# Performance work log

Hardware: AMD Instinct MI355X
Metric: run time of the kernel (lower is better)

The kernel has to match this reference:

```python
import jax, jax.numpy as jnp
import numpy as np

B, T, IN_CH, FIRST_CH, BLOCK_CH, SCALED_CH, K, ND = 8, 16384, 256, 256, 24, 128, 2, 10


def _conv1d(x, W, b, d=1):
    # x: (B, L, Cin), W: (K, Cin, Cout), keras Conv1D with padding='valid'
    y = jax.lax.conv_general_dilated(x, W, (1,), 'VALID', rhs_dilation=(d,),
                                     dimension_numbers=('NWC', 'WIO', 'NWC'))
    return y + b


def _gated(x, gW, gb, fW, fb, sW, sb, d):
    g = jax.nn.sigmoid(_conv1d(x, gW, gb, d))
    f = jnp.tanh(_conv1d(x, fW, fb, d))
    return _conv1d(f * g, sW, sb, 1)


def setup_inputs():
    key = jax.random.key(0)
    ks = jax.random.split(key, 11)
    s = 0.1
    n9 = ND - 1  # blocks 1..9 share channel count BLOCK_CH -> stacked weights
    return {
        'x': jax.random.normal(ks[0], (B, T, IN_CH), jnp.float32),
        'causal_W': jax.random.normal(ks[1], (K, IN_CH, FIRST_CH)) * s,
        'causal_b': jnp.zeros((FIRST_CH,)),
        'gW0': jax.random.normal(ks[2], (K, FIRST_CH, BLOCK_CH)) * s,
        'gb0': jnp.zeros((BLOCK_CH,)),
        'fW0': jax.random.normal(ks[3], (K, FIRST_CH, BLOCK_CH)) * s,
        'fb0': jnp.zeros((BLOCK_CH,)),
        'sW0': jax.random.normal(ks[4], (1, BLOCK_CH, BLOCK_CH)) * s,
        'sb0': jnp.zeros((BLOCK_CH,)),
        'gate_W': jax.random.normal(ks[5], (n9, K, BLOCK_CH, BLOCK_CH)) * s,
        'gate_b': jnp.zeros((n9, BLOCK_CH)),
        'filter_W': jax.random.normal(ks[6], (n9, K, BLOCK_CH, BLOCK_CH)) * s,
        'filter_b': jnp.zeros((n9, BLOCK_CH)),
        'scale_W': jax.random.normal(ks[7], (n9, 1, BLOCK_CH, BLOCK_CH)) * s,
        'scale_b': jnp.zeros((n9, BLOCK_CH)),
        'res_W': jax.random.normal(ks[8], (n9, 1, BLOCK_CH, SCALED_CH)) * s,
        'res_b': jnp.zeros((n9, SCALED_CH)),
        'f1_W': jax.random.normal(ks[9], (1, SCALED_CH, IN_CH)) * s,
        'f1_b': jnp.zeros((IN_CH,)),
        'f2_W': jax.random.normal(ks[10], (1, IN_CH, IN_CH)) * s,
        'f2_b': jnp.zeros((IN_CH,)),
    }


def reference(x, causal_W, causal_b, gW0, gb0, fW0, fb0, sW0, sb0,
              gate_W, gate_b, filter_W, filter_b, scale_W, scale_b,
              res_W, res_b, f1_W, f1_b, f2_W, f2_b):
    out = _conv1d(x, causal_W, causal_b)  # (B, T-1, 256)
    # block 0 (dilation 1): prev_in has 256 ch vs 24 ch out -> residual branch skipped
    out = _gated(out, gW0, gb0, fW0, fb0, sW0, sb0, 1)
    acc = None
    for i in range(ND - 1):
        d = 2 ** (i + 1)  # even -> trim d//2 on each side
        prev = out
        out = _gated(prev, gate_W[i], gate_b[i], filter_W[i], filter_b[i],
                     scale_W[i], scale_b[i], d)
        trimmed = prev[:, d // 2: prev.shape[1] - d // 2, :]
        # NOTE: original code OVERWRITES the accumulator each iteration
        acc = _conv1d(trimmed + out, res_W[i], res_b[i], 1)
    a = jax.nn.relu(acc)  # (B, 15360, 128)
    a = jax.nn.relu(_conv1d(a, f1_W, f1_b, 1))  # (B, 15360, 256)
    return jax.nn.softmax(_conv1d(a, f2_W, f2_b, 1), axis=-1)
```

## Files before the change

kernel.cpp:

```cpp
#include <hip/hip_runtime.h>
#include <math.h>

typedef unsigned short u16;
typedef __attribute__((ext_vector_type(8))) short short8;
typedef __attribute__((ext_vector_type(4))) float f32x4;

#define PBSTR ((long)16382 * 24)

__device__ __forceinline__ u16 f2bf(float f) {
    unsigned u = __float_as_uint(f);
    unsigned r = u + 0x7FFFu + ((u >> 16) & 1u);
    return (u16)(r >> 16);
}
__device__ __forceinline__ unsigned pk2(float a, float b) {
    return (unsigned)f2bf(a) | ((unsigned)f2bf(b) << 16);
}
__device__ __forceinline__ float sigf(float x) { return 1.f / (1.f + __expf(-x)); }
__device__ __forceinline__ float tanhfast(float x) { return 2.f / (1.f + __expf(-2.f * x)) - 1.f; }

__device__ __forceinline__ short8 ldfrag(const u16* p) { return *(const short8*)p; }
__device__ __forceinline__ short8 ldfrag(const float* p) {
    float4 v0 = *(const float4*)p;
    float4 v1 = *(const float4*)(p + 4);
    union { uint4 u; short8 s; } cv;
    cv.u.x = pk2(v0.x, v0.y); cv.u.y = pk2(v0.z, v0.w);
    cv.u.z = pk2(v1.x, v1.y); cv.u.w = pk2(v1.z, v1.w);
    return cv.s;
}

__global__ __launch_bounds__(256) void build_gf_w(
    const float* __restrict__ cW, const float* __restrict__ cb,
    const float* __restrict__ gW, const float* __restrict__ gb,
    const float* __restrict__ fW, const float* __restrict__ fb,
    u16* __restrict__ Wt, float* __restrict__ biasGF)
{
    int idx = blockIdx.x * 256 + threadIdx.x;
    if (idx < 49152) {
        int nr = idx / 768, k = idx % 768, tau = k / 256, ci = k % 256;
        float val = 0.f;
        if (nr < 48) {
            const float* G = (nr < 24) ? gW : fW;
            int n = (nr < 24) ? nr : nr - 24;
            auto dotf = [&](int i, int j) {
                const float* a = cW + i * 65536 + ci * 256;
                const float* g = G + j * 6144 + n;
                float s = 0.f;
                for (int o = 0; o < 256; ++o) s += a[o] * g[o * 24];
                return s;
            };
            if (tau == 0)      val = dotf(0, 0);
            else if (tau == 1) val = dotf(0, 1) + dotf(1, 0);
            else               val = dotf(1, 1);
        }
        Wt[idx] = f2bf(val);
    }
    if (blockIdx.x == 0 && threadIdx.x < 48) {
        int nr = threadIdx.x;
        const float* G = (nr < 24) ? gW : fW;
        const float* B = (nr < 24) ? gb : fb;
        int n = (nr < 24) ? nr : nr - 24;
        float s = B[n];
        for (int o = 0; o < 256; ++o) s += cb[o] * (G[o * 24 + n] + G[6144 + o * 24 + n]);
        biasGF[nr] = s;
    }
}

__global__ __launch_bounds__(256) void build_wt_misc(
    const float* __restrict__ f1W, const float* __restrict__ f2W,
    const float* __restrict__ resW8,
    const float* __restrict__ gateW, const float* __restrict__ filtW,
    const float* __restrict__ sclW,
    u16* __restrict__ Wt1, u16* __restrict__ Wt2, u16* __restrict__ Wtr,
    u16* __restrict__ Wgf, u16* __restrict__ Wsc)
{
    int idx = blockIdx.x * 256 + threadIdx.x;
    if (idx < 32768) {
        int n = idx / 128, k = idx % 128;
        Wt1[idx] = f2bf(f1W[k * 256 + n]);
    } else if (idx < 98304) {
        int j = idx - 32768; int n = j / 256, k = j % 256;
        Wt2[j] = f2bf(f2W[k * 256 + n]);
    } else if (idx < 102400) {
        int j = idx - 98304; int n = j / 32, k = j % 32;
        Wtr[j] = (k < 24) ? f2bf(resW8[k * 128 + n]) : (u16)0;
    } else if (idx < 130048) {
        int j = idx - 102400;
        int i = j / 3072, r = (j % 3072) / 64, k = j % 64;
        float v = 0.f;
        int tap = -1, ci = 0;
        if (k < 24) { tap = 0; ci = k; }
        else if (k >= 32 && k < 56) { tap = 1; ci = k - 32; }
        if (tap >= 0) {
            const float* W = (r < 24) ? gateW : filtW;
            int co = (r < 24) ? r : r - 24;
            v = W[((i * 2 + tap) * 24 + ci) * 24 + co];
        }
        Wgf[j] = f2bf(v);
    } else if (idx < 139264) {
        int j = idx - 130048;
        int i = j / 1024, r = (j % 1024) / 32, k = j % 32;
        float v = (r < 24 && k < 24) ? sclW[(i * 24 + k) * 24 + r] : 0.f;
        Wsc[j] = f2bf(v);
    }
}

template<typename AT, int KTOT, int NTILES, int ACT>
__global__ __launch_bounds__(256) void gemm_bstat(
    const AT* __restrict__ A, long A_bstride, int A_rs,
    const u16* __restrict__ Wt, int Wt_rs,
    const float* __restrict__ bias,
    u16* __restrict__ C, long C_bstride, int C_rs, int L_out)
{
    constexpr int BS = KTOT + 8;
    constexpr int NROWS = NTILES * 16;
    __shared__ __align__(16) u16 Bs[NROWS * BS];
    __shared__ float biasL[NROWS];
    const int tid = threadIdx.x;
    const int n0 = blockIdx.y * NROWS;

    for (int i = tid; i < NROWS * (KTOT / 8); i += 256) {
        int rn = i / (KTOT / 8), kk = i % (KTOT / 8);
        *(uint4*)&Bs[rn * BS + kk * 8] = *(const uint4*)(Wt + (long)(n0 + rn) * Wt_rs + kk * 8);
    }
    if (tid < NROWS) biasL[tid] = bias[n0 + tid];

    const int wv = tid >> 6, lane = tid & 63, col = lane & 15, quad = lane >> 4;
    const int b = blockIdx.z;
    const int m0 = blockIdx.x * 128 + wv * 32;
    const AT* Ab = A + (long)b * A_bstride;
    const int rmax = L_out - 1;

    f32x4 acc[2][NTILES];
#pragma unroll
    for (int i = 0; i < 2; ++i)
#pragma unroll
        for (int j = 0; j < NTILES; ++j) acc[i][j] = (f32x4){0.f, 0.f, 0.f, 0.f};

    __syncthreads();

#pragma unroll
    for (int k0 = 0; k0 < KTOT; k0 += 32) {
        short8 a[2];
#pragma unroll
        for (int mt = 0; mt < 2; ++mt) {
            int r = m0 + mt * 16 + col;
            if (r > rmax) r = rmax;
            a[mt] = ldfrag(Ab + (long)r * A_rs + k0 + quad * 8);
        }
#pragma unroll
        for (int nt = 0; nt < NTILES; ++nt) {
            short8 bb = *(const short8*)&Bs[(nt * 16 + col) * BS + k0 + quad * 8];
            acc[0][nt] = __builtin_amdgcn_mfma_f32_16x16x32_bf16(a[0], bb, acc[0][nt], 0, 0, 0);
            acc[1][nt] = __builtin_amdgcn_mfma_f32_16x16x32_bf16(a[1], bb, acc[1][nt], 0, 0, 0);
        }
    }

#pragma unroll
    for (int mt = 0; mt < 2; ++mt)
#pragma unroll
        for (int nt = 0; nt < NTILES; ++nt)
#pragma unroll
            for (int rr = 0; rr < 4; ++rr) {
                int t = m0 + mt * 16 + quad * 4 + rr;
                if (t < L_out) {
                    float v = acc[mt][nt][rr] + biasL[nt * 16 + col];
                    if (ACT == 1) v = fmaxf(v, 0.f);
                    C[(long)b * C_bstride + (long)t * C_rs + n0 + nt * 16 + col] = f2bf(v);
                }
            }
}

__global__ __launch_bounds__(256) void gf_fused_v3(
    const float* __restrict__ x, const u16* __restrict__ Wt,
    const float* __restrict__ biasGF,
    const float* __restrict__ sW, const float* __restrict__ sb,
    float* __restrict__ P)
{
    __shared__ __align__(16) union {
        u16 bs[48 * 392];
        struct { float pre[128 * 49]; float h[128 * 24]; } ep;
    } U;
    __shared__ float WsT[24 * 28];
    __shared__ float biasL[48];
    __shared__ float sbL[24];

    const int tid = threadIdx.x;
    const int m0 = blockIdx.x * 128;
    const int b = blockIdx.z;
    const float* xb = x + (long)b * (16384 * 256);
    const int L = 16382;

    for (int i = tid; i < 576; i += 256) { int c = i / 24, n = i % 24; WsT[n * 28 + c] = sW[i]; }
    if (tid < 48) biasL[tid] = biasGF[tid];
    if (tid < 24) sbL[tid] = sb[tid];

    const int wv = tid >> 6, lane = tid & 63, col = lane & 15, quad = lane >> 4;

    f32x4 acc[2][3];
#pragma unroll
    for (int i = 0; i < 2; ++i)
#pragma unroll
        for (int j = 0; j < 3; ++j) acc[i][j] = (f32x4){0.f, 0.f, 0.f, 0.f};

    for (int half = 0; half < 2; ++half) {
        if (half) __syncthreads();
        for (int i = tid; i < 2304; i += 256) {
            int rn = i / 48, kk = i % 48;
            *(uint4*)&U.bs[rn * 392 + kk * 8] =
                *(const uint4*)(Wt + (long)rn * 768 + half * 384 + kk * 8);
        }
        __syncthreads();

        for (int k0 = 0; k0 < 384; k0 += 32) {
            short8 a[2];
#pragma unroll
            for (int mt = 0; mt < 2; ++mt) {
                int g = m0 + wv * 32 + mt * 16 + col;
                if (g > 16381) g = 16381;
                a[mt] = ldfrag(xb + (long)g * 256 + half * 384 + k0 + quad * 8);
            }
#pragma unroll
            for (int nt = 0; nt < 3; ++nt) {
                short8 bb = *(const short8*)&U.bs[(nt * 16 + col) * 392 + k0 + quad * 8];
                acc[0][nt] = __builtin_amdgcn_mfma_f32_16x16x32_bf16(a[0], bb, acc[0][nt], 0, 0, 0);
                acc[1][nt] = __builtin_amdgcn_mfma_f32_16x16x32_bf16(a[1], bb, acc[1][nt], 0, 0, 0);
            }
        }
    }

    __syncthreads();
#pragma unroll
    for (int mt = 0; mt < 2; ++mt)
#pragma unroll
        for (int nt = 0; nt < 3; ++nt)
#pragma unroll
            for (int rr = 0; rr < 4; ++rr) {
                int lrow = wv * 32 + mt * 16 + quad * 4 + rr;
                int c = nt * 16 + col;
                U.ep.pre[lrow * 49 + c] = acc[mt][nt][rr] + biasL[c];
            }
    __syncthreads();
    for (int i = tid; i < 3072; i += 256) {
        int t = i / 24, c = i - t * 24;
        U.ep.h[t * 24 + c] = sigf(U.ep.pre[t * 49 + c]) * tanhfast(U.ep.pre[t * 49 + 24 + c]);
    }
    __syncthreads();
    {
        int t = tid >> 1, half = tid & 1;
        float hv[24];
#pragma unroll
        for (int q = 0; q < 6; ++q) {
            float4 v = *(const float4*)&U.ep.h[t * 24 + q * 4];
            hv[q * 4] = v.x; hv[q * 4 + 1] = v.y; hv[q * 4 + 2] = v.z; hv[q * 4 + 3] = v.w;
        }
        if (m0 + t < L) {
#pragma unroll
            for (int j = 0; j < 12; ++j) {
                int n = half * 12 + j;
                float o = sbL[n];
#pragma unroll
                for (int q = 0; q < 6; ++q) {
                    float4 w = *(const float4*)&WsT[n * 28 + q * 4];
                    o += hv[q*4] * w.x + hv[q*4+1] * w.y + hv[q*4+2] * w.z + hv[q*4+3] * w.w;
                }
                P[(long)b * PBSTR + (long)(m0 + t) * 24 + n] = o;
            }
        }
    }
}

__global__ __launch_bounds__(256) void gated_mfma(
    const float* __restrict__ Pin,
    const u16* __restrict__ WgfG, const float* __restrict__ gb,
    const float* __restrict__ fb,
    const u16* __restrict__ WsG, const float* __restrict__ sb,
    float* __restrict__ Q, int Lin, int Lout, int d, int trimOff)
{
    __shared__ __align__(16) union {
        u16 T[64 * 72];
        float pre[64 * 49];
    } U;
    __shared__ __align__(16) u16 Wgf[48 * 72];
    __shared__ __align__(16) u16 Ws[32 * 40];
    __shared__ __align__(16) u16 H[64 * 40];

    const int tid = threadIdx.x;
    const int m0 = blockIdx.x * 64;
    const int b = blockIdx.z;
    const float* Pb = Pin + (long)b * PBSTR;

    if (tid < 128) {
        int r = tid & 63, tap = tid >> 6;
        int t = m0 + r; if (t > Lout - 1) t = Lout - 1;
        const float* src = Pb + (long)(t + tap * d) * 24;
        u16* dst = &U.T[r * 72 + tap * 32];
#pragma unroll
        for (int q = 0; q < 3; ++q) {
            float4 va = *(const float4*)(src + q * 8);
            float4 vb = *(const float4*)(src + q * 8 + 4);
            uint4 u;
            u.x = pk2(va.x, va.y); u.y = pk2(va.z, va.w);
            u.z = pk2(vb.x, vb.y); u.w = pk2(vb.z, vb.w);
            *(uint4*)(dst + q * 8) = u;
        }
        *(uint4*)(dst + 24) = (uint4){0, 0, 0, 0};
    } else {
        for (int j = tid - 128; j < 384; j += 128) {
            int rn = j >> 3, kk = j & 7;
            *(uint4*)&Wgf[rn * 72 + kk * 8] = *(const uint4*)(WgfG + rn * 64 + kk * 8);
        }
        {
            int j = tid - 128;
            int rn = j >> 2, kk = j & 3;
            *(uint4*)&Ws[rn * 40 + kk * 8] = *(const uint4*)(WsG + rn * 32 + kk * 8);
        }
    }

    const int wv = tid >> 6, lane = tid & 63, col = lane & 15, quad = lane >> 4;

    __syncthreads();

    short8 bgf[2][3];
#pragma unroll
    for (int ks = 0; ks < 2; ++ks)
#pragma unroll
        for (int nt = 0; nt < 3; ++nt)
            bgf[ks][nt] = *(const short8*)&Wgf[(nt * 16 + col) * 72 + ks * 32 + quad * 8];

    short8 a0 = *(const short8*)&U.T[(wv * 16 + col) * 72 + quad * 8];
    short8 a1 = *(const short8*)&U.T[(wv * 16 + col) * 72 + 32 + quad * 8];

    f32x4 acc[3];
#pragma unroll
    for (int nt = 0; nt < 3; ++nt) acc[nt] = (f32x4){0.f, 0.f, 0.f, 0.f};
#pragma unroll
    for (int nt = 0; nt < 3; ++nt) {
        acc[nt] = __builtin_amdgcn_mfma_f32_16x16x32_bf16(a0, bgf[0][nt], acc[nt], 0, 0, 0);
        acc[nt] = __builtin_amdgcn_mfma_f32_16x16x32_bf16(a1, bgf[1][nt], acc[nt], 0, 0, 0);
    }

    __syncthreads();

    float bnt[3];
#pragma unroll
    for (int nt = 0; nt < 3; ++nt) {
        int n = nt * 16 + col;
        bnt[nt] = (n < 24) ? gb[n] : fb[n - 24];
    }
#pragma unroll
    for (int nt = 0; nt < 3; ++nt)
#pragma unroll
        for (int rr = 0; rr < 4; ++rr)
            U.pre[(wv * 16 + quad * 4 + rr) * 49 + nt * 16 + col] = acc[nt][rr] + bnt[nt];
    __syncthreads();

    for (int i2 = tid; i2 < 1536; i2 += 256) {
        int t = i2 / 24, c = i2 - t * 24;
        float g = U.pre[t * 49 + c], f = U.pre[t * 49 + 24 + c];
        H[t * 40 + c] = f2bf(sigf(g) * tanhfast(f));
    }
    for (int i2 = tid; i2 < 512; i2 += 256) {
        int t = i2 >> 3, c = i2 & 7;
        H[t * 40 + 24 + c] = 0;
    }
    __syncthreads();

    short8 aH = *(const short8*)&H[(wv * 16 + col) * 40 + quad * 8];
    f32x4 acc2[2];
#pragma unroll
    for (int nt = 0; nt < 2; ++nt) acc2[nt] = (f32x4){0.f, 0.f, 0.f, 0.f};
#pragma unroll
    for (int nt = 0; nt < 2; ++nt) {
        short8 bs2 = *(const short8*)&Ws[(nt * 16 + col) * 40 + quad * 8];
        acc2[nt] = __builtin_amdgcn_mfma_f32_16x16x32_bf16(aH, bs2, acc2[nt], 0, 0, 0);
    }

#pragma unroll
    for (int nt = 0; nt < 2; ++nt) {
        int n = nt * 16 + col;
        if (n < 24) {
            float sbn = sb[n];
#pragma unroll
            for (int rr = 0; rr < 4; ++rr) {
                int t = m0 + wv * 16 + quad * 4 + rr;
                if (t < Lout) {
                    float v = acc2[nt][rr] + sbn;
                    if (trimOff >= 0) v += Pb[(long)(t + trimOff) * 24 + n];
                    Q[(long)b * PBSTR + (long)t * 24 + n] = v;
                }
            }
        }
    }
}

__global__ __launch_bounds__(256) void f2_softmax_v2(
    const u16* __restrict__ A, const u16* __restrict__ Wt2,
    const float* __restrict__ bias, float* __restrict__ out)
{
    __shared__ __align__(16) u16 Bs[2][256 * 40];
    __shared__ float biasL[256];
    const int tid = threadIdx.x;
    const int b = blockIdx.y;
    const int t0 = blockIdx.x * 64;
    biasL[tid] = bias[tid];

    const int wv = tid >> 6, lane = tid & 63, col = lane & 15, quad = lane >> 4;
    const u16* Ab = A + (long)b * (15360L * 256);
    const int row = t0 + wv * 16 + col;

    auto stage = [&](int kc, int buf) {
#pragma unroll
        for (int j = 0; j < 4; ++j) {
            int idx = tid * 4 + j;
            int rn = idx >> 2, kk = idx & 3;
            *(uint4*)&Bs[buf][rn * 40 + kk * 8] =
                *(const uint4*)(Wt2 + (long)rn * 256 + kc * 32 + kk * 8);
        }
    };

    short8 afr[8];
#pragma unroll
    for (int kc = 0; kc < 8; ++kc)
        afr[kc] = *(const short8*)(Ab + (long)row * 256 + kc * 32 + quad * 8);

    f32x4 acc[16];
#pragma unroll
    for (int i = 0; i < 16; ++i) acc[i] = (f32x4){0.f, 0.f, 0.f, 0.f};

    stage(0, 0);
    __syncthreads();
    for (int kc = 0; kc < 8; ++kc) {
        int buf = kc & 1;
        if (kc < 7) stage(kc + 1, buf ^ 1);
#pragma unroll
        for (int nt = 0; nt < 16; ++nt) {
            short8 bb = *(const short8*)&Bs[buf][(nt * 16 + col) * 40 + quad * 8];
            acc[nt] = __builtin_amdgcn_mfma_f32_16x16x32_bf16(afr[kc], bb, acc[nt], 0, 0, 0);
        }
        __syncthreads();
    }

#pragma unroll
    for (int r = 0; r < 4; ++r) {
        int tl = wv * 16 + quad * 4 + r;
        float v[16];
        float m = -1e30f;
#pragma unroll
        for (int nt = 0; nt < 16; ++nt) {
            v[nt] = acc[nt][r] + biasL[nt * 16 + col];
            m = fmaxf(m, v[nt]);
        }
        m = fmaxf(m, __shfl_xor(m, 1));
        m = fmaxf(m, __shfl_xor(m, 2));
        m = fmaxf(m, __shfl_xor(m, 4));
        m = fmaxf(m, __shfl_xor(m, 8));
        float s = 0.f;
#pragma unroll
        for (int nt = 0; nt < 16; ++nt) { v[nt] = __expf(v[nt] - m); s += v[nt]; }
        s += __shfl_xor(s, 1);
        s += __shfl_xor(s, 2);
        s += __shfl_xor(s, 4);
        s += __shfl_xor(s, 8);
        float inv = 1.f / s;
        float* op = out + ((long)b * 15360 + t0 + tl) * 256;
#pragma unroll
        for (int nt = 0; nt < 16; ++nt) op[nt * 16 + col] = v[nt] * inv;
    }
}

extern "C" void kernel_launch(void* const* d_in, const int* in_sizes, int n_in,
                              void* d_out, int out_size, void* d_ws, size_t ws_size,
                              hipStream_t stream)
{
    const float* x        = (const float*)d_in[0];
    const float* causal_W = (const float*)d_in[1];
    const float* causal_b = (const float*)d_in[2];
    const float* gW0      = (const float*)d_in[3];
    const float* gb0      = (const float*)d_in[4];
    const float* fW0      = (const float*)d_in[5];
    const float* fb0      = (const float*)d_in[6];
    const float* sW0      = (const float*)d_in[7];
    const float* sb0      = (const float*)d_in[8];
    const float* gate_W   = (const float*)d_in[9];
    const float* gate_b   = (const float*)d_in[10];
    const float* filter_W = (const float*)d_in[11];
    const float* filter_b = (const float*)d_in[12];
    const float* scale_W  = (const float*)d_in[13];
    const float* scale_b  = (const float*)d_in[14];
    const float* res_W    = (const float*)d_in[15];
    const float* res_b    = (const float*)d_in[16];
    const float* f1_W     = (const float*)d_in[17];
    const float* f1_b     = (const float*)d_in[18];
    const float* f2_W     = (const float*)d_in[19];
    const float* f2_b     = (const float*)d_in[20];

    char* w = (char*)d_ws;
    u16* ACC  = (u16*)w;   w += (size_t)8 * 15360 * 128 * 2;
    u16* A1   = (u16*)w;   w += (size_t)8 * 15360 * 256 * 2;
    float* P0 = (float*)w; w += (size_t)8 * 16382 * 24 * 4;
    float* P1 = (float*)w; w += (size_t)8 * 16382 * 24 * 4;
    u16* WtGF = (u16*)w;   w += (size_t)64 * 768 * 2;
    u16* Wt1  = (u16*)w;   w += (size_t)256 * 128 * 2;
    u16* Wt2  = (u16*)w;   w += (size_t)256 * 256 * 2;
    u16* Wtr  = (u16*)w;   w += (size_t)128 * 32 * 2;
    float* biasGF = (float*)w; w += 256;
    u16* WgfG = (u16*)w;   w += (size_t)9 * 48 * 64 * 2;
    u16* WsG  = (u16*)w;   w += (size_t)9 * 32 * 32 * 2;

    dim3 blk(256);

    build_gf_w<<<dim3(192), blk, 0, stream>>>(causal_W, causal_b, gW0, gb0, fW0, fb0,
                                              WtGF, biasGF);
    build_wt_misc<<<dim3(544), blk, 0, stream>>>(f1_W, f2_W, res_W + (size_t)8 * 24 * 128,
                                                 gate_W, filter_W, scale_W,
                                                 Wt1, Wt2, Wtr, WgfG, WsG);

    gf_fused_v3<<<dim3(128, 1, 8), blk, 0, stream>>>(x, WtGF, biasGF, sW0, sb0, P0);

    float* Pprev = P0;
    float* Pnext = P1;
    int Lprev = 16382;
    for (int i = 0; i < 9; ++i) {
        int d = 2 << i;
        int L = Lprev - d;
        int trim = (i == 8) ? d / 2 : -1;
        gated_mfma<<<dim3((L + 63) / 64, 1, 8), blk, 0, stream>>>(
            Pprev, WgfG + (size_t)i * 3072, gate_b + i * 24, filter_b + i * 24,
            WsG + (size_t)i * 1024, scale_b + i * 24,
            Pnext, Lprev, L, d, trim);
        float* tmp = Pprev; Pprev = Pnext; Pnext = tmp;
        Lprev = L;
    }

    gemm_bstat<float, 32, 8, 1><<<dim3(120, 1, 8), blk, 0, stream>>>(
        Pprev, PBSTR, 24, Wtr, 32, res_b + 8 * 128,
        ACC, (long)15360 * 128, 128, 15360);

    gemm_bstat<u16, 128, 8, 1><<<dim3(120, 2, 8), blk, 0, stream>>>(
        ACC, (long)15360 * 128, 128, Wt1, 128, f1_b,
        A1, (long)15360 * 256, 256, 15360);

    f2_softmax_v2<<<dim3(240, 8), blk, 0, stream>>>(A1, Wt2, f2_b, (float*)d_out);
}
```

Measured before the change: 577.5 us.

## Store gated-block intermediates as bf16 and prefetch A fragments in GEMMs

The 24-channel intermediate buffers P0/P1 passed between the gated blocks now hold bf16 instead of fp32. Every gated block reads them with plain vector copies into shared memory instead of converting from fp32, which halves intermediate traffic. The first fused kernel double-buffers its fp32 x loads in registers ahead of the MFMA loop, and gemm_bstat loads all A fragments up front before the MFMA loop. The cost is an extra bf16 rounding on each residual path across ten chained layers, plus higher register pressure from the prefetch buffers.

```diff
diff --git a/kernel.cpp b/kernel.cpp
--- a/kernel.cpp
+++ b/kernel.cpp
@@ -12,6 +12,7 @@
     unsigned r = u + 0x7FFFu + ((u >> 16) & 1u);
     return (u16)(r >> 16);
 }
+__device__ __forceinline__ float bf2f(u16 v) { return __uint_as_float((unsigned)v << 16); }
 __device__ __forceinline__ unsigned pk2(float a, float b) {
     return (unsigned)f2bf(a) | ((unsigned)f2bf(b) << 16);
 }
@@ -25,6 +26,12 @@
     union { uint4 u; short8 s; } cv;
     cv.u.x = pk2(v0.x, v0.y); cv.u.y = pk2(v0.z, v0.w);
     cv.u.z = pk2(v1.x, v1.y); cv.u.w = pk2(v1.z, v1.w);
+    return cv.s;
+}
+__device__ __forceinline__ short8 cvt8(float4 lo, float4 hi) {
+    union { uint4 u; short8 s; } cv;
+    cv.u.x = pk2(lo.x, lo.y); cv.u.y = pk2(lo.z, lo.w);
+    cv.u.z = pk2(hi.x, hi.y); cv.u.w = pk2(hi.z, hi.w);
     return cv.s;
 }
 
@@ -113,6 +120,7 @@
 {
     constexpr int BS = KTOT + 8;
     constexpr int NROWS = NTILES * 16;
+    constexpr int KS = KTOT / 32;
     __shared__ __align__(16) u16 Bs[NROWS * BS];
     __shared__ float biasL[NROWS];
     const int tid = threadIdx.x;
@@ -130,28 +138,31 @@
     const AT* Ab = A + (long)b * A_bstride;
     const int rmax = L_out - 1;
 
-    f32x4 acc[2][NTILES];
-#pragma unroll
-    for (int i = 0; i < 2; ++i)
-#pragma unroll
-        for (int j = 0; j < NTILES; ++j) acc[i][j] = (f32x4){0.f, 0.f, 0.f, 0.f};
-
-    __syncthreads();
-
-#pragma unroll
-    for (int k0 = 0; k0 < KTOT; k0 += 32) {
-        short8 a[2];
+    short8 afr[KS][2];
+#pragma unroll
+    for (int ks = 0; ks < KS; ++ks)
 #pragma unroll
         for (int mt = 0; mt < 2; ++mt) {
             int r = m0 + mt * 16 + col;
             if (r > rmax) r = rmax;
-            a[mt] = ldfrag(Ab + (long)r * A_rs + k0 + quad * 8);
-        }
+            afr[ks][mt] = ldfrag(Ab + (long)r * A_rs + ks * 32 + quad * 8);
+        }
+
+    f32x4 acc[2][NTILES];
+#pragma unroll
+    for (int i = 0; i < 2; ++i)
+#pragma unroll
+        for (int j = 0; j < NTILES; ++j) acc[i][j] = (f32x4){0.f, 0.f, 0.f, 0.f};
+
+    __syncthreads();
+
+#pragma unroll
+    for (int ks = 0; ks < KS; ++ks) {
 #pragma unroll
         for (int nt = 0; nt < NTILES; ++nt) {
-            short8 bb = *(const short8*)&Bs[(nt * 16 + col) * BS + k0 + quad * 8];
-            acc[0][nt] = __builtin_amdgcn_mfma_f32_16x16x32_bf16(a[0], bb, acc[0][nt], 0, 0, 0);
-            acc[1][nt] = __builtin_amdgcn_mfma_f32_16x16x32_bf16(a[1], bb, acc[1][nt], 0, 0, 0);
+            short8 bb = *(const short8*)&Bs[(nt * 16 + col) * BS + ks * 32 + quad * 8];
+            acc[0][nt] = __builtin_amdgcn_mfma_f32_16x16x32_bf16(afr[ks][0], bb, acc[0][nt], 0, 0, 0);
+            acc[1][nt] = __builtin_amdgcn_mfma_f32_16x16x32_bf16(afr[ks][1], bb, acc[1][nt], 0, 0, 0);
         }
     }
 
@@ -170,11 +181,11 @@
             }
 }
 
-__global__ __launch_bounds__(256) void gf_fused_v3(
+__global__ __launch_bounds__(256) void gf_fused_v4(
     const float* __restrict__ x, const u16* __restrict__ Wt,
     const float* __restrict__ biasGF,
     const float* __restrict__ sW, const float* __restrict__ sb,
-    float* __restrict__ P)
+    u16* __restrict__ P)
 {
     __shared__ __align__(16) union {
         u16 bs[48 * 392];
@@ -196,12 +207,34 @@
 
     const int wv = tid >> 6, lane = tid & 63, col = lane & 15, quad = lane >> 4;
 
+    long rowoff[2];
+#pragma unroll
+    for (int mt = 0; mt < 2; ++mt) {
+        int g = m0 + wv * 32 + mt * 16 + col;
+        if (g > 16381) g = 16381;
+        rowoff[mt] = (long)g * 256 + quad * 8;
+    }
+
+    float4 pf[2][2][2];
+    auto loadA = [&](int kk, int slot) {
+#pragma unroll
+        for (int mt = 0; mt < 2; ++mt) {
+            const float* p = xb + rowoff[mt] + kk * 32;
+            pf[slot][mt][0] = *(const float4*)p;
+            pf[slot][mt][1] = *(const float4*)(p + 4);
+        }
+    };
+
     f32x4 acc[2][3];
 #pragma unroll
     for (int i = 0; i < 2; ++i)
 #pragma unroll
         for (int j = 0; j < 3; ++j) acc[i][j] = (f32x4){0.f, 0.f, 0.f, 0.f};
 
+    loadA(0, 0);
+    loadA(1, 1);
+
+#pragma unroll
     for (int half = 0; half < 2; ++half) {
         if (half) __syncthreads();
         for (int i = tid; i < 2304; i += 256) {
@@ -211,19 +244,18 @@
         }
         __syncthreads();
 
-        for (int k0 = 0; k0 < 384; k0 += 32) {
-            short8 a[2];
-#pragma unroll
-            for (int mt = 0; mt < 2; ++mt) {
-                int g = m0 + wv * 32 + mt * 16 + col;
-                if (g > 16381) g = 16381;
-                a[mt] = ldfrag(xb + (long)g * 256 + half * 384 + k0 + quad * 8);
-            }
+#pragma unroll
+        for (int s = 0; s < 12; ++s) {
+            const int kk = half * 12 + s;
+            const int slot = s & 1;
+            short8 a0 = cvt8(pf[slot][0][0], pf[slot][0][1]);
+            short8 a1 = cvt8(pf[slot][1][0], pf[slot][1][1]);
+            if (kk + 2 < 24) loadA(kk + 2, slot);
 #pragma unroll
             for (int nt = 0; nt < 3; ++nt) {
-                short8 bb = *(const short8*)&U.bs[(nt * 16 + col) * 392 + k0 + quad * 8];
-                acc[0][nt] = __builtin_amdgcn_mfma_f32_16x16x32_bf16(a[0], bb, acc[0][nt], 0, 0, 0);
-                acc[1][nt] = __builtin_amdgcn_mfma_f32_16x16x32_bf16(a[1], bb, acc[1][nt], 0, 0, 0);
+                short8 bb = *(const short8*)&U.bs[(nt * 16 + col) * 392 + s * 32 + quad * 8];
+                acc[0][nt] = __builtin_amdgcn_mfma_f32_16x16x32_bf16(a0, bb, acc[0][nt], 0, 0, 0);
+                acc[1][nt] = __builtin_amdgcn_mfma_f32_16x16x32_bf16(a1, bb, acc[1][nt], 0, 0, 0);
             }
         }
     }
@@ -263,18 +295,18 @@
                     float4 w = *(const float4*)&WsT[n * 28 + q * 4];
                     o += hv[q*4] * w.x + hv[q*4+1] * w.y + hv[q*4+2] * w.z + hv[q*4+3] * w.w;
                 }
-                P[(long)b * PBSTR + (long)(m0 + t) * 24 + n] = o;
+                P[(long)b * PBSTR + (long)(m0 + t) * 24 + n] = f2bf(o);
             }
         }
     }
 }
 
 __global__ __launch_bounds__(256) void gated_mfma(
-    const float* __restrict__ Pin,
+    const u16* __restrict__ Pin,
     const u16* __restrict__ WgfG, const float* __restrict__ gb,
     const float* __restrict__ fb,
     const u16* __restrict__ WsG, const float* __restrict__ sb,
-    float* __restrict__ Q, int Lin, int Lout, int d, int trimOff)
+    u16* __restrict__ Q, int Lin, int Lout, int d, int trimOff)
 {
     __shared__ __align__(16) union {
         u16 T[64 * 72];
@@ -287,22 +319,16 @@
     const int tid = threadIdx.x;
     const int m0 = blockIdx.x * 64;
     const int b = blockIdx.z;
-    const float* Pb = Pin + (long)b * PBSTR;
+    const u16* Pb = Pin + (long)b * PBSTR;
 
     if (tid < 128) {
         int r = tid & 63, tap = tid >> 6;
         int t = m0 + r; if (t > Lout - 1) t = Lout - 1;
-        const float* src = Pb + (long)(t + tap * d) * 24;
+        const u16* src = Pb + (long)(t + tap * d) * 24;
         u16* dst = &U.T[r * 72 + tap * 32];
-#pragma unroll
-        for (int q = 0; q < 3; ++q) {
-            float4 va = *(const float4*)(src + q * 8);
-            float4 vb = *(const float4*)(src + q * 8 + 4);
-            uint4 u;
-            u.x = pk2(va.x, va.y); u.y = pk2(va.z, va.w);
-            u.z = pk2(vb.x, vb.y); u.w = pk2(vb.z, vb.w);
-            *(uint4*)(dst + q * 8) = u;
-        }
+        *(uint4*)(dst)      = *(const uint4*)(src);
+        *(uint4*)(dst + 8)  = *(const uint4*)(src + 8);
+        *(uint4*)(dst + 16) = *(const uint4*)(src + 16);
         *(uint4*)(dst + 24) = (uint4){0, 0, 0, 0};
     } else {
         for (int j = tid - 128; j < 384; j += 128) {
@@ -385,8 +411,8 @@
                 int t = m0 + wv * 16 + quad * 4 + rr;
                 if (t < Lout) {
                     float v = acc2[nt][rr] + sbn;
-                    if (trimOff >= 0) v += Pb[(long)(t + trimOff) * 24 + n];
-                    Q[(long)b * PBSTR + (long)t * 24 + n] = v;
+                    if (trimOff >= 0) v += bf2f(Pb[(long)(t + trimOff) * 24 + n]);
+                    Q[(long)b * PBSTR + (long)t * 24 + n] = f2bf(v);
                 }
             }
         }
@@ -497,8 +523,8 @@
     char* w = (char*)d_ws;
     u16* ACC  = (u16*)w;   w += (size_t)8 * 15360 * 128 * 2;
     u16* A1   = (u16*)w;   w += (size_t)8 * 15360 * 256 * 2;
-    float* P0 = (float*)w; w += (size_t)8 * 16382 * 24 * 4;
-    float* P1 = (float*)w; w += (size_t)8 * 16382 * 24 * 4;
+    u16* P0   = (u16*)w;   w += (size_t)8 * 16382 * 24 * 2;
+    u16* P1   = (u16*)w;   w += (size_t)8 * 16382 * 24 * 2;
     u16* WtGF = (u16*)w;   w += (size_t)64 * 768 * 2;
     u16* Wt1  = (u16*)w;   w += (size_t)256 * 128 * 2;
     u16* Wt2  = (u16*)w;   w += (size_t)256 * 256 * 2;
@@ -515,10 +541,10 @@
                                                  gate_W, filter_W, scale_W,
                                                  Wt1, Wt2, Wtr, WgfG, WsG);
 
-    gf_fused_v3<<<dim3(128, 1, 8), blk, 0, stream>>>(x, WtGF, biasGF, sW0, sb0, P0);
-
-    float* Pprev = P0;
-    float* Pnext = P1;
+    gf_fused_v4<<<dim3(128, 1, 8), blk, 0, stream>>>(x, WtGF, biasGF, sW0, sb0, P0);
+
+    u16* Pprev = P0;
+    u16* Pnext = P1;
     int Lprev = 16382;
     for (int i = 0; i < 9; ++i) {
         int d = 2 << i;
@@ -528,11 +554,11 @@
             Pprev, WgfG + (size_t)i * 3072, gate_b + i * 24, filter_b + i * 24,
             WsG + (size_t)i * 1024, scale_b + i * 24,
             Pnext, Lprev, L, d, trim);
-        float* tmp = Pprev; Pprev = Pnext; Pnext = tmp;
+        u16* tmp = Pprev; Pprev = Pnext; Pnext = tmp;
         Lprev = L;
     }
 
-    gemm_bstat<float, 32, 8, 1><<<dim3(120, 1, 8), blk, 0, stream>>>(
+    gemm_bstat<u16, 32, 8, 1><<<dim3(120, 1, 8), blk, 0, stream>>>(
         Pprev, PBSTR, 24, Wtr, 32, res_b + 8 * 128,
         ACC, (long)15360 * 128, 128, 15360);
 
```

New measurement: 569.9 us. No clear change (-1.3%).

## Fuse nine dilated gated blocks into one LDS-resident kernel with bf16 intermediates

Applied to the files above, without the earlier changes.

Replaces the nine per-layer gated_mfma launches with a single gated_stack kernel. Each block loads a 256-row output tile plus a 1022-row halo of the block-0 output into LDS and runs all nine dilated gated layers in place, writing only the final trimmed result. Intermediates are stored as bf16 instead of fp32. The residual GEMM now preloads all A fragments before the MFMA loop. This removes eight launches and their global round trips, at the cost of recomputing the halo in every tile, holding about 62KB of LDS per block with few blocks per CU, and serializing the layers inside each block with barriers.

```diff
diff --git a/kernel.cpp b/kernel.cpp
--- a/kernel.cpp
+++ b/kernel.cpp
@@ -6,12 +6,14 @@
 typedef __attribute__((ext_vector_type(4))) float f32x4;
 
 #define PBSTR ((long)16382 * 24)
+#define PFSTR ((long)15360 * 24)
 
 __device__ __forceinline__ u16 f2bf(float f) {
     unsigned u = __float_as_uint(f);
     unsigned r = u + 0x7FFFu + ((u >> 16) & 1u);
     return (u16)(r >> 16);
 }
+__device__ __forceinline__ float bf2f(u16 v) { return __uint_as_float((unsigned)v << 16); }
 __device__ __forceinline__ unsigned pk2(float a, float b) {
     return (unsigned)f2bf(a) | ((unsigned)f2bf(b) << 16);
 }
@@ -113,6 +115,7 @@
 {
     constexpr int BS = KTOT + 8;
     constexpr int NROWS = NTILES * 16;
+    constexpr int KS = KTOT / 32;
     __shared__ __align__(16) u16 Bs[NROWS * BS];
     __shared__ float biasL[NROWS];
     const int tid = threadIdx.x;
@@ -130,28 +133,31 @@
     const AT* Ab = A + (long)b * A_bstride;
     const int rmax = L_out - 1;
 
-    f32x4 acc[2][NTILES];
-#pragma unroll
-    for (int i = 0; i < 2; ++i)
-#pragma unroll
-        for (int j = 0; j < NTILES; ++j) acc[i][j] = (f32x4){0.f, 0.f, 0.f, 0.f};
-
-    __syncthreads();
-
-#pragma unroll
-    for (int k0 = 0; k0 < KTOT; k0 += 32) {
-        short8 a[2];
+    short8 afr[KS][2];
+#pragma unroll
+    for (int ks = 0; ks < KS; ++ks)
 #pragma unroll
         for (int mt = 0; mt < 2; ++mt) {
             int r = m0 + mt * 16 + col;
             if (r > rmax) r = rmax;
-            a[mt] = ldfrag(Ab + (long)r * A_rs + k0 + quad * 8);
-        }
+            afr[ks][mt] = ldfrag(Ab + (long)r * A_rs + ks * 32 + quad * 8);
+        }
+
+    f32x4 acc[2][NTILES];
+#pragma unroll
+    for (int i = 0; i < 2; ++i)
+#pragma unroll
+        for (int j = 0; j < NTILES; ++j) acc[i][j] = (f32x4){0.f, 0.f, 0.f, 0.f};
+
+    __syncthreads();
+
+#pragma unroll
+    for (int ks = 0; ks < KS; ++ks) {
 #pragma unroll
         for (int nt = 0; nt < NTILES; ++nt) {
-            short8 bb = *(const short8*)&Bs[(nt * 16 + col) * BS + k0 + quad * 8];
-            acc[0][nt] = __builtin_amdgcn_mfma_f32_16x16x32_bf16(a[0], bb, acc[0][nt], 0, 0, 0);
-            acc[1][nt] = __builtin_amdgcn_mfma_f32_16x16x32_bf16(a[1], bb, acc[1][nt], 0, 0, 0);
+            short8 bb = *(const short8*)&Bs[(nt * 16 + col) * BS + ks * 32 + quad * 8];
+            acc[0][nt] = __builtin_amdgcn_mfma_f32_16x16x32_bf16(afr[ks][0], bb, acc[0][nt], 0, 0, 0);
+            acc[1][nt] = __builtin_amdgcn_mfma_f32_16x16x32_bf16(afr[ks][1], bb, acc[1][nt], 0, 0, 0);
         }
     }
 
@@ -170,11 +176,11 @@
             }
 }
 
-__global__ __launch_bounds__(256) void gf_fused_v3(
+__global__ __launch_bounds__(256) void gf_fused_v5(
     const float* __restrict__ x, const u16* __restrict__ Wt,
     const float* __restrict__ biasGF,
     const float* __restrict__ sW, const float* __restrict__ sb,
-    float* __restrict__ P)
+    u16* __restrict__ P)
 {
     __shared__ __align__(16) union {
         u16 bs[48 * 392];
@@ -263,133 +269,117 @@
                     float4 w = *(const float4*)&WsT[n * 28 + q * 4];
                     o += hv[q*4] * w.x + hv[q*4+1] * w.y + hv[q*4+2] * w.z + hv[q*4+3] * w.w;
                 }
-                P[(long)b * PBSTR + (long)(m0 + t) * 24 + n] = o;
-            }
-        }
-    }
-}
-
-__global__ __launch_bounds__(256) void gated_mfma(
-    const float* __restrict__ Pin,
-    const u16* __restrict__ WgfG, const float* __restrict__ gb,
-    const float* __restrict__ fb,
-    const u16* __restrict__ WsG, const float* __restrict__ sb,
-    float* __restrict__ Q, int Lin, int Lout, int d, int trimOff)
-{
-    __shared__ __align__(16) union {
-        u16 T[64 * 72];
-        float pre[64 * 49];
-    } U;
-    __shared__ __align__(16) u16 Wgf[48 * 72];
-    __shared__ __align__(16) u16 Ws[32 * 40];
-    __shared__ __align__(16) u16 H[64 * 40];
+                P[(long)b * PBSTR + (long)(m0 + t) * 24 + n] = f2bf(o);
+            }
+        }
+    }
+}
+
+__global__ __launch_bounds__(256) void gated_stack(
+    const u16* __restrict__ P0,
+    const u16* __restrict__ WgfG, const u16* __restrict__ WsG,
+    const float* __restrict__ gateB, const float* __restrict__ filtB,
+    const float* __restrict__ sclB,
+    u16* __restrict__ Pfin)
+{
+    __shared__ __align__(16) u16 buf[1296 * 24];
+    __shared__ __align__(16) u16 hs[2][64 * 40];
 
     const int tid = threadIdx.x;
-    const int m0 = blockIdx.x * 64;
-    const int b = blockIdx.z;
-    const float* Pb = Pin + (long)b * PBSTR;
-
+    const int wv = tid >> 6, lane = tid & 63, col = lane & 15, quad = lane >> 4;
+    const int m0 = blockIdx.x * 256;
+    const int b  = blockIdx.z;
+
+    {
+        const u16* src = P0 + (long)b * PBSTR + (long)m0 * 24;
+        for (int j = tid; j < 3888; j += 256) {
+            uint4 v = (j < 3834) ? *(const uint4*)(src + j * 8) : (uint4){0, 0, 0, 0};
+            *(uint4*)&buf[j * 8] = v;
+        }
+    }
     if (tid < 128) {
-        int r = tid & 63, tap = tid >> 6;
-        int t = m0 + r; if (t > Lout - 1) t = Lout - 1;
-        const float* src = Pb + (long)(t + tap * d) * 24;
-        u16* dst = &U.T[r * 72 + tap * 32];
-#pragma unroll
-        for (int q = 0; q < 3; ++q) {
-            float4 va = *(const float4*)(src + q * 8);
-            float4 vb = *(const float4*)(src + q * 8 + 4);
-            uint4 u;
-            u.x = pk2(va.x, va.y); u.y = pk2(va.z, va.w);
-            u.z = pk2(vb.x, vb.y); u.w = pk2(vb.z, vb.w);
-            *(uint4*)(dst + q * 8) = u;
-        }
-        *(uint4*)(dst + 24) = (uint4){0, 0, 0, 0};
-    } else {
-        for (int j = tid - 128; j < 384; j += 128) {
-            int rn = j >> 3, kk = j & 7;
-            *(uint4*)&Wgf[rn * 72 + kk * 8] = *(const uint4*)(WgfG + rn * 64 + kk * 8);
-        }
-        {
-            int j = tid - 128;
-            int rn = j >> 2, kk = j & 3;
-            *(uint4*)&Ws[rn * 40 + kk * 8] = *(const uint4*)(WsG + rn * 32 + kk * 8);
-        }
-    }
-
-    const int wv = tid >> 6, lane = tid & 63, col = lane & 15, quad = lane >> 4;
-
+        int bu = tid >> 6, r = tid & 63;
+        *(uint4*)&hs[bu][r * 40 + 24] = (uint4){0, 0, 0, 0};
+    }
     __syncthreads();
 
-    short8 bgf[2][3];
-#pragma unroll
-    for (int ks = 0; ks < 2; ++ks)
-#pragma unroll
-        for (int nt = 0; nt < 3; ++nt)
-            bgf[ks][nt] = *(const short8*)&Wgf[(nt * 16 + col) * 72 + ks * 32 + quad * 8];
-
-    short8 a0 = *(const short8*)&U.T[(wv * 16 + col) * 72 + quad * 8];
-    short8 a1 = *(const short8*)&U.T[(wv * 16 + col) * 72 + 32 + quad * 8];
-
-    f32x4 acc[3];
-#pragma unroll
-    for (int nt = 0; nt < 3; ++nt) acc[nt] = (f32x4){0.f, 0.f, 0.f, 0.f};
-#pragma unroll
-    for (int nt = 0; nt < 3; ++nt) {
-        acc[nt] = __builtin_amdgcn_mfma_f32_16x16x32_bf16(a0, bgf[0][nt], acc[nt], 0, 0, 0);
-        acc[nt] = __builtin_amdgcn_mfma_f32_16x16x32_bf16(a1, bgf[1][nt], acc[nt], 0, 0, 0);
-    }
-
-    __syncthreads();
-
-    float bnt[3];
-#pragma unroll
-    for (int nt = 0; nt < 3; ++nt) {
-        int n = nt * 16 + col;
-        bnt[nt] = (n < 24) ? gb[n] : fb[n - 24];
-    }
-#pragma unroll
-    for (int nt = 0; nt < 3; ++nt)
-#pragma unroll
-        for (int rr = 0; rr < 4; ++rr)
-            U.pre[(wv * 16 + quad * 4 + rr) * 49 + nt * 16 + col] = acc[nt][rr] + bnt[nt];
-    __syncthreads();
-
-    for (int i2 = tid; i2 < 1536; i2 += 256) {
-        int t = i2 / 24, c = i2 - t * 24;
-        float g = U.pre[t * 49 + c], f = U.pre[t * 49 + 24 + c];
-        H[t * 40 + c] = f2bf(sigf(g) * tanhfast(f));
-    }
-    for (int i2 = tid; i2 < 512; i2 += 256) {
-        int t = i2 >> 3, c = i2 & 7;
-        H[t * 40 + 24 + c] = 0;
-    }
-    __syncthreads();
-
-    short8 aH = *(const short8*)&H[(wv * 16 + col) * 40 + quad * 8];
-    f32x4 acc2[2];
-#pragma unroll
-    for (int nt = 0; nt < 2; ++nt) acc2[nt] = (f32x4){0.f, 0.f, 0.f, 0.f};
-#pragma unroll
-    for (int nt = 0; nt < 2; ++nt) {
-        short8 bs2 = *(const short8*)&Ws[(nt * 16 + col) * 40 + quad * 8];
-        acc2[nt] = __builtin_amdgcn_mfma_f32_16x16x32_bf16(aH, bs2, acc2[nt], 0, 0, 0);
-    }
-
-#pragma unroll
-    for (int nt = 0; nt < 2; ++nt) {
-        int n = nt * 16 + col;
-        if (n < 24) {
-            float sbn = sb[n];
+    int W = 1278;
+    int hb = 0;
+    for (int li = 0; li < 9; ++li) {
+        const int d = 2 << li;
+        const int Wn = W - d;
+        const bool last = (li == 8);
+
+        const u16* wg = WgfG + li * 3072;
+        short8 bgf0[3], bgf1[3];
+#pragma unroll
+        for (int nt = 0; nt < 3; ++nt) {
+            bgf0[nt] = *(const short8*)(wg + (nt * 16 + col) * 64 + quad * 8);
+            bgf1[nt] = *(const short8*)(wg + (nt * 16 + col) * 64 + 32 + quad * 8);
+        }
+        const u16* wsp = WsG + li * 1024;
+        short8 wsf0 = *(const short8*)(wsp + col * 32 + quad * 8);
+        short8 wsf1 = *(const short8*)(wsp + (16 + col) * 32 + quad * 8);
+        const float bv0 = gateB[li * 24 + col];
+        const float bv1 = (col < 8) ? gateB[li * 24 + 16 + col] : filtB[li * 24 + col - 8];
+        const float bv2 = filtB[li * 24 + 8 + col];
+        const float sv0 = sclB[li * 24 + col];
+        const float sv1 = (col < 8) ? sclB[li * 24 + 16 + col] : 0.f;
+
+        for (int c = 0; c < Wn; c += 64) {
+            const int r0 = c + wv * 16 + col;
+            short8 a0 = *(const short8*)&buf[r0 * 24 + quad * 8];
+            short8 a1 = *(const short8*)&buf[(r0 + d) * 24 + quad * 8];
+            f32x4 ac0 = {0.f, 0.f, 0.f, 0.f}, ac1 = ac0, ac2 = ac0;
+            ac0 = __builtin_amdgcn_mfma_f32_16x16x32_bf16(a0, bgf0[0], ac0, 0, 0, 0);
+            ac0 = __builtin_amdgcn_mfma_f32_16x16x32_bf16(a1, bgf1[0], ac0, 0, 0, 0);
+            ac1 = __builtin_amdgcn_mfma_f32_16x16x32_bf16(a0, bgf0[1], ac1, 0, 0, 0);
+            ac1 = __builtin_amdgcn_mfma_f32_16x16x32_bf16(a1, bgf1[1], ac1, 0, 0, 0);
+            ac2 = __builtin_amdgcn_mfma_f32_16x16x32_bf16(a0, bgf0[2], ac2, 0, 0, 0);
+            ac2 = __builtin_amdgcn_mfma_f32_16x16x32_bf16(a1, bgf1[2], ac2, 0, 0, 0);
+
+            const int lr = wv * 16 + quad * 4;
+            u16* hp = &hs[hb][0];
 #pragma unroll
             for (int rr = 0; rr < 4; ++rr) {
-                int t = m0 + wv * 16 + quad * 4 + rr;
-                if (t < Lout) {
-                    float v = acc2[nt][rr] + sbn;
-                    if (trimOff >= 0) v += Pb[(long)(t + trimOff) * 24 + n];
-                    Q[(long)b * PBSTR + (long)t * 24 + n] = v;
+                float g0 = ac0[rr] + bv0;
+                float m1 = ac1[rr] + bv1;
+                float m2 = ac2[rr] + bv2;
+                float s1 = __shfl_xor(m1, 8);
+                float s2 = __shfl_xor(m2, 8);
+                float f0 = (col < 8) ? s1 : s2;
+                hp[(lr + rr) * 40 + col] = f2bf(sigf(g0) * tanhfast(f0));
+                if (col < 8)
+                    hp[(lr + rr) * 40 + 16 + col] = f2bf(sigf(m1) * tanhfast(s2));
+            }
+            __syncthreads();
+
+            short8 aH = *(const short8*)&hp[(wv * 16 + col) * 40 + quad * 8];
+            f32x4 c0 = {0.f, 0.f, 0.f, 0.f}, c1 = c0;
+            c0 = __builtin_amdgcn_mfma_f32_16x16x32_bf16(aH, wsf0, c0, 0, 0, 0);
+            c1 = __builtin_amdgcn_mfma_f32_16x16x32_bf16(aH, wsf1, c1, 0, 0, 0);
+#pragma unroll
+            for (int rr = 0; rr < 4; ++rr) {
+                int t = c + wv * 16 + quad * 4 + rr;
+                float v0 = c0[rr] + sv0;
+                if (last) v0 += bf2f(buf[(t + 256) * 24 + col]);
+                buf[t * 24 + col] = f2bf(v0);
+                if (col < 8) {
+                    float v1 = c1[rr] + sv1;
+                    if (last) v1 += bf2f(buf[(t + 256) * 24 + 16 + col]);
+                    buf[t * 24 + 16 + col] = f2bf(v1);
                 }
             }
-        }
+            hb ^= 1;
+        }
+        __syncthreads();
+        W = Wn;
+    }
+
+    {
+        u16* dst = Pfin + (long)b * PFSTR + (long)m0 * 24;
+        for (int j = tid; j < 768; j += 256)
+            *(uint4*)(dst + j * 8) = *(const uint4*)&buf[j * 8];
     }
 }
 
@@ -497,8 +487,8 @@
     char* w = (char*)d_ws;
     u16* ACC  = (u16*)w;   w += (size_t)8 * 15360 * 128 * 2;
     u16* A1   = (u16*)w;   w += (size_t)8 * 15360 * 256 * 2;
-    float* P0 = (float*)w; w += (size_t)8 * 16382 * 24 * 4;
-    float* P1 = (float*)w; w += (size_t)8 * 16382 * 24 * 4;
+    u16* P0   = (u16*)w;   w += (size_t)8 * 16382 * 24 * 2;
+    u16* Pfin = (u16*)w;   w += (size_t)8 * 15360 * 24 * 2 + 128;
     u16* WtGF = (u16*)w;   w += (size_t)64 * 768 * 2;
     u16* Wt1  = (u16*)w;   w += (size_t)256 * 128 * 2;
     u16* Wt2  = (u16*)w;   w += (size_t)256 * 256 * 2;
@@ -515,25 +505,13 @@
                                                  gate_W, filter_W, scale_W,
                                                  Wt1, Wt2, Wtr, WgfG, WsG);
 
-    gf_fused_v3<<<dim3(128, 1, 8), blk, 0, stream>>>(x, WtGF, biasGF, sW0, sb0, P0);
-
-    float* Pprev = P0;
-    float* Pnext = P1;
-    int Lprev = 16382;
-    for (int i = 0; i < 9; ++i) {
-        int d = 2 << i;
-        int L = Lprev - d;
-        int trim = (i == 8) ? d / 2 : -1;
-        gated_mfma<<<dim3((L + 63) / 64, 1, 8), blk, 0, stream>>>(
-            Pprev, WgfG + (size_t)i * 3072, gate_b + i * 24, filter_b + i * 24,
-            WsG + (size_t)i * 1024, scale_b + i * 24,
-            Pnext, Lprev, L, d, trim);
-        float* tmp = Pprev; Pprev = Pnext; Pnext = tmp;
-        Lprev = L;
-    }
-
-    gemm_bstat<float, 32, 8, 1><<<dim3(120, 1, 8), blk, 0, stream>>>(
-        Pprev, PBSTR, 24, Wtr, 32, res_b + 8 * 128,
+    gf_fused_v5<<<dim3(128, 1, 8), blk, 0, stream>>>(x, WtGF, biasGF, sW0, sb0, P0);
+
+    gated_stack<<<dim3(60, 1, 8), blk, 0, stream>>>(P0, WgfG, WsG,
+                                                    gate_b, filter_b, scale_b, Pfin);
+
+    gemm_bstat<u16, 32, 8, 1><<<dim3(120, 1, 8), blk, 0, stream>>>(
+        Pfin, PFSTR, 24, Wtr, 32, res_b + 8 * 128,
         ACC, (long)15360 * 128, 128, 15360);
 
     gemm_bstat<u16, 128, 8, 1><<<dim3(120, 2, 8), blk, 0, stream>>>(
```

New measurement: 696.4 us. 1.21x slower.
